# Kernel tuning notes

Measured on AMD Instinct MI355X. Metric: run time of the kernel, lower is better.

## Reference

```python
import jax, jax.numpy as jnp
from jax import lax
import numpy as np

# --- module constants (from init_kwargs) ---
MAXK = 512
BLOCK = 3            # Shi-Tomasi structure-tensor window
NUM_PAIRS = 256      # BAD descriptor dimensionality
ITERS = 20           # Sinkhorn iterations
EPS = 1.0            # entropy regularization
UNUSED = 1.0         # dustbin score
NMS_R = 3
THR = 0.0
PATCH_R = 8          # BAD pair-offset radius
BOX = 5              # BAD pre-smoothing box size

# fixed BAD comparison-pair offsets (dy1,dx1,dy2,dx2) -- constants, not learned
_OFFSETS = jnp.asarray(
    np.random.RandomState(42).randint(-PATCH_R, PATCH_R + 1, size=(NUM_PAIRS, 4)),
    dtype=jnp.int32)

_SOBEL_X = jnp.array([[-1., 0., 1.], [-2., 0., 2.], [-1., 0., 1.]], jnp.float32)[None, None]
_SOBEL_Y = jnp.transpose(_SOBEL_X, (0, 1, 3, 2))


def _conv(x, k):  # x: [B,1,H,W], k: [1,1,kh,kw]
    return lax.conv_general_dilated(x, k, (1, 1), 'SAME',
                                    dimension_numbers=('NCHW', 'OIHW', 'NCHW'))


def _detector(img):
    """Shi-Tomasi min-eigenvalue score map + dense BAD descriptor map."""
    Ix = _conv(img, _SOBEL_X)
    Iy = _conv(img, _SOBEL_Y)
    box = jnp.ones((1, 1, BLOCK, BLOCK), jnp.float32) / (BLOCK * BLOCK)
    Ixx = _conv(Ix * Ix, box)
    Iyy = _conv(Iy * Iy, box)
    Ixy = _conv(Ix * Iy, box)
    score = 0.5 * ((Ixx + Iyy) - jnp.sqrt((Ixx - Iyy) ** 2 + 4.0 * Ixy ** 2 + 1e-12))

    smooth = _conv(img, jnp.ones((1, 1, BOX, BOX), jnp.float32) / (BOX * BOX))[:, 0]  # [B,H,W]
    B, H, W = smooth.shape
    pad = jnp.pad(smooth, ((0, 0), (PATCH_R, PATCH_R), (PATCH_R, PATCH_R)), mode='edge')

    def one_pair(off):  # box-average difference at two shifted locations
        a = lax.dynamic_slice(pad, (0, PATCH_R + off[0], PATCH_R + off[1]), (B, H, W))
        b = lax.dynamic_slice(pad, (0, PATCH_R + off[2], PATCH_R + off[3]), (B, H, W))
        return a - b

    desc = jax.vmap(one_pair)(_OFFSETS)           # [D,B,H,W]
    return score[:, 0], jnp.transpose(desc, (1, 0, 2, 3))  # [B,H,W], [B,D,H,W]


def _nms_topk(score):
    """Max-pool NMS + top-k keypoint selection; invalid kpts = (-1,-1)."""
    win = 2 * NMS_R + 1
    mx = lax.reduce_window(score, -jnp.inf, lax.max, (1, win, win), (1, 1, 1), 'SAME')
    mask = (score >= mx) & (score > THR)
    B, H, W = score.shape
    masked = jnp.where(mask, score, -jnp.inf).reshape(B, H * W)
    vals, idx = lax.top_k(masked, MAXK)
    valid = jnp.isfinite(vals)
    y = (idx // W).astype(jnp.float32)
    x = (idx % W).astype(jnp.float32)
    kpts = jnp.where(valid[..., None], jnp.stack([y, x], -1), -1.0)  # [B,K,2] (y,x)
    return kpts


def _extract(desc_map, kpts):
    """Bilinear (subpixel) descriptor gather; zeros for invalid keypoints."""
    B, D, H, W = desc_map.shape
    valid = (kpts[:, :, 0] >= 0).astype(desc_map.dtype)
    y = jnp.clip(kpts[:, :, 0], 0.0, H - 1.0)
    x = jnp.clip(kpts[:, :, 1], 0.0, W - 1.0)
    y0 = jnp.floor(y); x0 = jnp.floor(x)
    y1 = jnp.minimum(y0 + 1.0, H - 1.0); x1 = jnp.minimum(x0 + 1.0, W - 1.0)
    wy = y - y0; wx = x - x0
    y0i, y1i = y0.astype(jnp.int32), y1.astype(jnp.int32)
    x0i, x1i = x0.astype(jnp.int32), x1.astype(jnp.int32)
    flat = desc_map.reshape(B, D, H * W)

    def g(yi, xi):  # [B,K] -> [B,D,K]
        return jnp.take_along_axis(flat, (yi * W + xi)[:, None, :], axis=2)

    d = (g(y0i, x0i) * ((1 - wy) * (1 - wx))[:, None, :]
         + g(y0i, x1i) * ((1 - wy) * wx)[:, None, :]
         + g(y1i, x0i) * (wy * (1 - wx))[:, None, :]
         + g(y1i, x1i) * (wy * wx)[:, None, :])
    return jnp.transpose(d, (0, 2, 1)) * valid[..., None]  # [B,K,D]


def _sinkhorn(d1, d2):
    """Log-domain Sinkhorn with dustbin row/col (SuperGlue-style OT)."""
    s1 = jnp.sum(d1 * d1, -1)
    s2 = jnp.sum(d2 * d2, -1)
    dist = jnp.sqrt(jnp.clip(
        s1[:, :, None] + s2[:, None, :] - 2.0 * jnp.einsum('bkd,bld->bkl', d1, d2),
        1e-12))
    B, K, _ = dist.shape
    Z = jnp.full((B, K + 1, K + 1), UNUSED / EPS, dtype=dist.dtype)
    Z = Z.at[:, :K, :K].set(-dist / EPS)
    norm = -jnp.log(2.0 * K)
    log_mu = jnp.concatenate([jnp.zeros((K,), Z.dtype),
                              jnp.log(jnp.full((1,), float(K), Z.dtype))]) + norm
    log_nu = log_mu

    def body(_, uv):
        u, v = uv
        u = log_mu - jax.scipy.special.logsumexp(Z + v[:, None, :], axis=2)
        v = log_nu - jax.scipy.special.logsumexp(Z + u[:, :, None], axis=1)
        return (u, v)

    u0 = jnp.zeros((B, K + 1), Z.dtype)
    u, v = lax.fori_loop(0, ITERS, body, (u0, u0))
    return jnp.exp(Z + u[:, :, None] + v[:, None, :] - norm)  # [B,K+1,K+1]


def _l2norm(d):
    return d / (jnp.linalg.norm(d, axis=-1, keepdims=True) + 1e-12)


def setup_inputs() -> dict:
    key = jax.random.key(0)
    k1, k2 = jax.random.split(key)
    image1 = jax.random.uniform(k1, (1, 1, 480, 640), jnp.float32)
    image2 = jax.random.uniform(k2, (1, 1, 480, 640), jnp.float32)
    return {"image1": image1, "image2": image2}


def reference(image1, image2):
    s1, m1 = _detector(image1)
    s2, m2 = _detector(image2)
    kpts1 = _nms_topk(s1)
    kpts2 = _nms_topk(s2)
    d1 = _l2norm(_extract(m1, kpts1))
    d2 = _l2norm(_extract(m2, kpts2))
    probs = _sinkhorn(d1, d2)
    return (kpts1, kpts2, probs)
```

## Files before the change

### kernel.cpp

```cpp
#include <hip/hip_runtime.h>
#include <math.h>
#include <stdint.h>

#define HH 480
#define WW 640
#define HW (HH*WW)
#define KK 512
#define DD 256
#define KP1 513
#define NSLOT 16
#define NBX 40
#define NBY 30
#define SLOTS_PER_IMG (NBX*NBY*NSLOT)
#define SVCAP 2048
#define SB 32
#define MU0 (1.0f/1024.0f)
#define MU1 (0.5f)
#define EDUST 2.71828182845904523536f

#define OFF_E      16384u
#define OFF_SMOOTH 2473984u
#define OFF_CAND   4931584u
#define OFF_KIDX   5238784u
#define OFF_DESC   5242880u
#define OFF_SBUF   6291456u
#define OFF_PC     6295552u
#define OFF_EU     6426880u

struct OffsTab { int v[1024]; };
static constexpr OffsTab make_offsets() {
  OffsTab o{};
  unsigned st[624] = {};
  st[0] = 42u;
  for (int i = 1; i < 624; ++i)
    st[i] = 1812433253u*(st[i-1] ^ (st[i-1] >> 30)) + (unsigned)i;
  int idx = 624, got = 0;
  while (got < 1024) {
    if (idx == 624) {
      for (int i = 0; i < 624; ++i) {
        unsigned y = (st[i] & 0x80000000u) | (st[(i+1)%624] & 0x7fffffffu);
        st[i] = st[(i+397)%624] ^ (y >> 1) ^ ((y & 1u) ? 2567483615u : 0u);
      }
      idx = 0;
    }
    unsigned y = st[idx++];
    y ^= y >> 11;
    y ^= (y << 7)  & 2636928640u;
    y ^= (y << 15) & 4022730752u;
    y ^= y >> 18;
    unsigned mv = y & 31u;
    if (mv <= 16u) { o.v[got] = (int)mv - 8; ++got; }
  }
  return o;
}
__device__ __constant__ OffsTab OFFS = make_offsets();

__global__ __launch_bounds__(256) void detnms_kernel(const float* __restrict__ img0,
    const float* __restrict__ img1, float* __restrict__ smooth,
    unsigned long long* __restrict__ cand) {
  __shared__ float tile[26][26];
  __shared__ float ixA[24][24], iyA[24][24];
  __shared__ float sc[22][22];
  __shared__ float vs[16][26];
  __shared__ float vm[16][22];
  __shared__ int wsum[4], wbase[4];
  const int imgI = blockIdx.z;
  const float* img = imgI ? img1 : img0;
  const int bx0 = blockIdx.x*16, by0 = blockIdx.y*16;
  const int tx = threadIdx.x, ty = threadIdx.y, lt = ty*16+tx;
  for (int p = lt; p < 676; p += 256) {
    int r = p/26, c = p%26;
    int gy = by0-5+r, gx = bx0-5+c;
    tile[r][c] = (gy >= 0 && gy < HH && gx >= 0 && gx < WW) ? img[gy*WW+gx] : 0.f;
  }
  __syncthreads();
  for (int p = lt; p < 576; p += 256) {
    int r = p/24, c = p%24;
    int gy = by0-4+r, gx = bx0-4+c;
    float ix = 0.f, iy = 0.f;
    if (gy >= 0 && gy < HH && gx >= 0 && gx < WW) {
      float t00 = tile[r][c],   t01 = tile[r][c+1],   t02 = tile[r][c+2];
      float t10 = tile[r+1][c],                        t12 = tile[r+1][c+2];
      float t20 = tile[r+2][c], t21 = tile[r+2][c+1], t22 = tile[r+2][c+2];
      ix = t00*(-1.f) + t02*1.f + t10*(-2.f) + t12*2.f + t20*(-1.f) + t22*1.f;
      iy = t00*(-1.f) + t01*(-2.f) + t02*(-1.f) + t20*1.f + t21*2.f + t22*1.f;
    }
    ixA[r][c] = ix; iyA[r][c] = iy;
  }
  __syncthreads();
  const float c9 = 1.f/9.f, c25 = 1.f/25.f;
  for (int p = lt; p < 484; p += 256) {
    int r = p/22, c = p%22;
    int gy = by0-3+r, gx = bx0-3+c;
    float v = -INFINITY;
    if (gy >= 0 && gy < HH && gx >= 0 && gx < WW) {
      float sxx = 0.f, syy = 0.f, sxy = 0.f;
      for (int dr = 0; dr < 3; ++dr)
        for (int dc = 0; dc < 3; ++dc) {
          float jx = ixA[r+dr][c+dc], jy = iyA[r+dr][c+dc];
          float pxxv = jx*jx, pyyv = jy*jy, pxyv = jx*jy;
          sxx += pxxv*c9; syy += pyyv*c9; sxy += pxyv*c9;
        }
      float tdif = sxx - syy;
      v = 0.5f * ((sxx + syy) - sqrtf(tdif*tdif + 4.f*(sxy*sxy) + 1e-12f));
    }
    sc[r][c] = v;
  }
  for (int p = lt; p < 416; p += 256) {
    int i = p/26, c = p%26;
    vs[i][c] = tile[i+3][c] + tile[i+4][c] + tile[i+5][c] + tile[i+6][c] + tile[i+7][c];
  }
  __syncthreads();
  for (int p = lt; p < 352; p += 256) {
    int i = p/22, c = p%22;
    float m = sc[i][c];
    m = fmaxf(m, sc[i+1][c]); m = fmaxf(m, sc[i+2][c]); m = fmaxf(m, sc[i+3][c]);
    m = fmaxf(m, sc[i+4][c]); m = fmaxf(m, sc[i+5][c]); m = fmaxf(m, sc[i+6][c]);
    vm[i][c] = m;
  }
  float sm = (vs[ty][tx+3] + vs[ty][tx+4] + vs[ty][tx+5] + vs[ty][tx+6] + vs[ty][tx+7]) * c25;
  smooth[imgI*HW + (by0+ty)*WW + (bx0+tx)] = sm;
  __syncthreads();
  float cv = sc[ty+3][tx+3];
  float m = vm[ty][tx];
  m = fmaxf(m, vm[ty][tx+1]); m = fmaxf(m, vm[ty][tx+2]); m = fmaxf(m, vm[ty][tx+3]);
  m = fmaxf(m, vm[ty][tx+4]); m = fmaxf(m, vm[ty][tx+5]); m = fmaxf(m, vm[ty][tx+6]);
  bool pred = (cv >= m && cv > 0.f);
  unsigned long long mask = __ballot(pred);
  int lane = lt & 63, wid = lt >> 6;
  if (lane == 0) wsum[wid] = __popcll(mask);
  __syncthreads();
  if (lt == 0) {
    int s0 = wsum[0], s1 = wsum[1], s2 = wsum[2], s3 = wsum[3];
    wbase[0] = 0; wbase[1] = s0; wbase[2] = s0+s1; wbase[3] = s0+s1+s2;
    wsum[0] = s0+s1+s2+s3;
  }
  __syncthreads();
  const int total = wsum[0];
  const size_t slotBase = (size_t)imgI*SLOTS_PER_IMG + (size_t)(blockIdx.y*NBX + blockIdx.x)*NSLOT;
  if (pred) {
    int pos = wbase[wid] + __popcll(mask & ((1ull << lane) - 1ull));
    if (pos < NSLOT) {
      int idx = (by0+ty)*WW + (bx0+tx);
      unsigned int ub = __float_as_uint(cv) | 0x80000000u;
      cand[slotBase + pos] = ((unsigned long long)ub << 32) | (unsigned int)(~idx);
    }
  }
  if (lt >= total && lt < NSLOT) cand[slotBase + lt] = 0ull;
}

__global__ __launch_bounds__(1024) void select2_kernel(const unsigned long long* __restrict__ cand,
    float* __restrict__ kptsOut, int* __restrict__ kidx) {
  __shared__ unsigned long long sk[SVCAP];
  __shared__ int hist[1024];
  __shared__ int sB1, sB2, sNeed, sCount;
  const int imgI = blockIdx.x, t = threadIdx.x;
  const unsigned long long* cd = cand + (size_t)imgI*SLOTS_PER_IMG;
  unsigned long long kreg[19];
  #pragma unroll
  for (int r = 0; r < 19; ++r) {
    int i = t + r*1024;
    kreg[r] = (i < SLOTS_PER_IMG) ? cd[i] : 0ull;
  }
  hist[t] = 0;
  if (t == 0) { sB1 = -1; sB2 = 0; sCount = 0; }
  __syncthreads();
  #pragma unroll
  for (int r = 0; r < 19; ++r)
    if (kreg[r]) atomicAdd(&hist[(int)(kreg[r] >> 54)], 1);
  __syncthreads();
  for (int d = 1; d < 1024; d <<= 1) {
    int vv = hist[t] + ((t + d < 1024) ? hist[t + d] : 0);
    __syncthreads();
    hist[t] = vv;
    __syncthreads();
  }
  if (hist[t] >= KK) atomicMax(&sB1, t);
  __syncthreads();
  const int b1 = sB1;
  if (t == 0 && b1 >= 0) sNeed = KK - ((b1 < 1023) ? hist[b1 + 1] : 0);
  __syncthreads();
  int b2 = 0;
  if (b1 >= 0) {
    hist[t] = 0;
    __syncthreads();
    #pragma unroll
    for (int r = 0; r < 19; ++r) {
      unsigned long long k = kreg[r];
      if (k && (int)(k >> 54) == b1) atomicAdd(&hist[(int)(k >> 44) & 1023], 1);
    }
    __syncthreads();
    for (int d = 1; d < 1024; d <<= 1) {
      int vv = hist[t] + ((t + d < 1024) ? hist[t + d] : 0);
      __syncthreads();
      hist[t] = vv;
      __syncthreads();
    }
    if (hist[t] >= sNeed) atomicMax(&sB2, t);
    __syncthreads();
    b2 = sB2;
  }
  #pragma unroll
  for (int r = 0; r < 19; ++r) {
    unsigned long long k = kreg[r];
    if (k) {
      int bin1 = (int)(k >> 54);
      if (bin1 > b1 || (bin1 == b1 && ((int)(k >> 44) & 1023) >= b2)) {
        int pos = atomicAdd(&sCount, 1);
        if (pos < SVCAP) sk[pos] = k;
      }
    }
  }
  __syncthreads();
  const int n = (sCount < SVCAP) ? sCount : SVCAP;
  for (int k = n + t; k < KK; k += 1024) {
    kptsOut[imgI*2*KK + 2*k]     = -1.f;
    kptsOut[imgI*2*KK + 2*k + 1] = -1.f;
    kidx[imgI*KK + k] = -1;
  }
  for (int i = t; i < n; i += 1024) {
    unsigned long long key = sk[i];
    int r = 0;
    for (int m = 0; m < n; ++m) r += (sk[m] > key) ? 1 : 0;
    if (r < KK) {
      int id = (int)(~(unsigned int)(key & 0xFFFFFFFFull));
      kptsOut[imgI*2*KK + 2*r]     = (float)(id / WW);
      kptsOut[imgI*2*KK + 2*r + 1] = (float)(id % WW);
      kidx[imgI*KK + r] = id;
    }
  }
}

__global__ __launch_bounds__(256) void desc_kernel(const float* __restrict__ smooth,
    const int* __restrict__ kidx, float* __restrict__ desc, float* __restrict__ sbuf) {
  __shared__ float wsum[4];
  const int k = blockIdx.x, imgI = blockIdx.y;
  const int j = threadIdx.x;
  const int id = kidx[imgI*KK + k];
  float val = 0.f;
  if (id >= 0) {
    int y = id / WW, x = id % WW;
    int o0 = OFFS.v[4*j], o1 = OFFS.v[4*j+1], o2 = OFFS.v[4*j+2], o3 = OFFS.v[4*j+3];
    const float* sm = smooth + imgI*HW;
    int ya = min(max(y+o0, 0), HH-1), xa = min(max(x+o1, 0), WW-1);
    int yb = min(max(y+o2, 0), HH-1), xb = min(max(x+o3, 0), WW-1);
    val = sm[ya*WW + xa] - sm[yb*WW + xb];
  }
  float ss = val*val;
  for (int off = 32; off; off >>= 1) ss += __shfl_down(ss, off);
  if ((j & 63) == 0) wsum[j >> 6] = ss;
  __syncthreads();
  if (j == 0) wsum[0] = wsum[0] + wsum[1] + wsum[2] + wsum[3];
  __syncthreads();
  float tot = wsum[0];
  float inv = 1.f / (sqrtf(tot) + 1e-12f);
  desc[((size_t)imgI*KK + k)*DD + j] = val * inv;
  if (j == 0) sbuf[imgI*KK + k] = tot * inv * inv;
}

__global__ __launch_bounds__(256) void zbuild_kernel(const float* __restrict__ desc,
    const float* __restrict__ sbuf, float* __restrict__ E) {
  __shared__ float sA[32][260], sB[32][260];
  const int ty = threadIdx.y, tx = threadIdx.x;
  const int i0 = blockIdx.y*32, j0 = blockIdx.x*32;
  const int lt = ty*16 + tx;
  for (int p = lt; p < 32*DD; p += 256) {
    int r = p >> 8, c = p & 255;
    sA[r][c] = desc[((size_t)(i0 + r))*DD + c];
    sB[r][c] = desc[((size_t)(KK + j0 + r))*DD + c];
  }
  __syncthreads();
  const float4* pa0 = (const float4*)&sA[ty][0];
  const float4* pa1 = (const float4*)&sA[ty+16][0];
  const float4* pb0 = (const float4*)&sB[tx][0];
  const float4* pb1 = (const float4*)&sB[tx+16][0];
  float a00 = 0.f, a01 = 0.f, a10 = 0.f, a11 = 0.f;
  for (int c4 = 0; c4 < DD/4; ++c4) {
    float4 a0 = pa0[c4], a1 = pa1[c4], b0 = pb0[c4], b1 = pb1[c4];
    a00 += a0.x*b0.x; a00 += a0.y*b0.y; a00 += a0.z*b0.z; a00 += a0.w*b0.w;
    a01 += a0.x*b1.x; a01 += a0.y*b1.y; a01 += a0.z*b1.z; a01 += a0.w*b1.w;
    a10 += a1.x*b0.x; a10 += a1.y*b0.y; a10 += a1.z*b0.z; a10 += a1.w*b0.w;
    a11 += a1.x*b1.x; a11 += a1.y*b1.y; a11 += a1.z*b1.z; a11 += a1.w*b1.w;
  }
  const float s0 = sbuf[i0 + ty], s0b = sbuf[i0 + ty + 16];
  const float s1 = sbuf[KK + j0 + tx], s1b = sbuf[KK + j0 + tx + 16];
  E[(size_t)(i0+ty)   *KK + j0+tx]    = expf(-sqrtf(fmaxf(s0  + s1  - 2.f*a00, 1e-12f)));
  E[(size_t)(i0+ty)   *KK + j0+tx+16] = expf(-sqrtf(fmaxf(s0  + s1b - 2.f*a01, 1e-12f)));
  E[(size_t)(i0+ty+16)*KK + j0+tx]    = expf(-sqrtf(fmaxf(s0b + s1  - 2.f*a10, 1e-12f)));
  E[(size_t)(i0+ty+16)*KK + j0+tx+16] = expf(-sqrtf(fmaxf(s0b + s1b - 2.f*a11, 1e-12f)));
}

__global__ __launch_bounds__(1024) void sink_step_kernel(const float* __restrict__ E,
    const float* __restrict__ PcolIn, float* __restrict__ PcolOut,
    float* __restrict__ euBuf, float* __restrict__ probs, int mode) {
  __shared__ float ev[KP1];
  __shared__ float pcolw[16][520];
  const int t = threadIdx.x, b = blockIdx.x;
  const int widx = t >> 6, lane = t & 63;
  const int r = b*16 + widx;
  const int j0 = lane*8;
  if (mode == 0) {
    for (int j = t; j < KP1; j += 1024) ev[j] = 1.f;
  } else {
    for (int j = t; j < KP1; j += 1024) {
      float s = 0.f;
      #pragma unroll
      for (int w = 0; w < SB; ++w) s += PcolIn[w*KP1 + j];
      float nu = (j < KK) ? MU0 : MU1;
      ev[j] = nu / s;
    }
  }
  __syncthreads();
  float4 va = *(const float4*)&ev[j0];
  float4 vb = *(const float4*)&ev[j0+4];
  float evv[8] = {va.x,va.y,va.z,va.w,vb.x,vb.y,vb.z,vb.w};
  const float ev512 = ev[512];
  const float* er = E + (size_t)r*KK;
  float4 e0 = *(const float4*)&er[j0];
  float4 e1 = *(const float4*)&er[j0+4];
  float ee[8] = {e0.x,e0.y,e0.z,e0.w,e1.x,e1.y,e1.z,e1.w};
  if (mode == 2) {
    const float euR = euBuf[r];
    float* pr = probs + (size_t)r*KP1;
    #pragma unroll
    for (int q = 0; q < 8; ++q) pr[j0+q] = ee[q] * euR * evv[q] * 1024.f;
    if (lane == 0) pr[512] = EDUST * euR * ev512 * 1024.f;
    if (r == 511) {
      const float euD = euBuf[512];
      float* pd = probs + (size_t)512*KP1;
      #pragma unroll
      for (int q = 0; q < 8; ++q) pd[j0+q] = EDUST * euD * evv[q] * 1024.f;
      if (lane == 0) pd[512] = EDUST * euD * ev512 * 1024.f;
    }
    return;
  }
  float S = 0.f;
  #pragma unroll
  for (int q = 0; q < 8; ++q) S += ee[q] * evv[q];
  if (lane == 0) S += EDUST * ev512;
  #pragma unroll
  for (int off = 32; off; off >>= 1) S += __shfl_xor(S, off);
  const float euR = MU0 / S;
  if (lane == 0) euBuf[r] = euR;
  float pacc[8];
  #pragma unroll
  for (int q = 0; q < 8; ++q) pacc[q] = ee[q] * euR;
  float pacc8 = EDUST * euR;
  if (r == 511) {
    float Sd = 0.f;
    #pragma unroll
    for (int q = 0; q < 8; ++q) Sd += evv[q];
    if (lane == 0) Sd += ev512;
    #pragma unroll
    for (int off = 32; off; off >>= 1) Sd += __shfl_xor(Sd, off);
    Sd *= EDUST;
    const float euD = MU1 / Sd;
    if (lane == 0) euBuf[512] = euD;
    #pragma unroll
    for (int q = 0; q < 8; ++q) pacc[q] += EDUST * euD;
    pacc8 += EDUST * euD;
  }
  *(float4*)&pcolw[widx][j0]   = make_float4(pacc[0], pacc[1], pacc[2], pacc[3]);
  *(float4*)&pcolw[widx][j0+4] = make_float4(pacc[4], pacc[5], pacc[6], pacc[7]);
  if (lane == 0) pcolw[widx][512] = pacc8;
  __syncthreads();
  float* pc = PcolOut + b*KP1;
  for (int j = t; j < KP1; j += 1024) {
    float s = 0.f;
    #pragma unroll
    for (int w = 0; w < 16; ++w) s += pcolw[w][j];
    pc[j] = s;
  }
}

extern "C" void kernel_launch(void* const* d_in, const int* in_sizes, int n_in,
                              void* d_out, int out_size, void* d_ws, size_t ws_size,
                              hipStream_t stream) {
  const float* img1 = (const float*)d_in[0];
  const float* img2 = (const float*)d_in[1];
  float* out = (float*)d_out;
  char* ws = (char*)d_ws;

  float* smooth = (float*)(ws + OFF_SMOOTH);
  unsigned long long* cand = (unsigned long long*)(ws + OFF_CAND);
  int*   kidx   = (int*)  (ws + OFF_KIDX);
  float* desc   = (float*)(ws + OFF_DESC);
  float* sbuf   = (float*)(ws + OFF_SBUF);
  float* E      = (float*)(ws + OFF_E);
  float* pcA    = (float*)(ws + OFF_PC);
  float* pcB    = (float*)(ws + OFF_PC) + SB*KP1;
  float* euBuf  = (float*)(ws + OFF_EU);
  float* probsOut = out + 2*KK*2;

  detnms_kernel<<<dim3(NBX, NBY, 2), dim3(16, 16), 0, stream>>>(img1, img2, smooth, cand);
  select2_kernel<<<2, 1024, 0, stream>>>(cand, out, kidx);
  desc_kernel<<<dim3(KK, 2), 256, 0, stream>>>(smooth, kidx, desc, sbuf);
  zbuild_kernel<<<dim3(16, 16), dim3(16, 16), 0, stream>>>(desc, sbuf, E);

  sink_step_kernel<<<SB, 1024, 0, stream>>>(E, pcB, pcA, euBuf, probsOut, 0);
  int ping = 0;
  for (int it = 1; it < 20; ++it) {
    float* pin  = ping ? pcB : pcA;
    float* pout = ping ? pcA : pcB;
    sink_step_kernel<<<SB, 1024, 0, stream>>>(E, pin, pout, euBuf, probsOut, 1);
    ping ^= 1;
  }
  {
    float* pin = ping ? pcB : pcA;
    sink_step_kernel<<<SB, 1024, 0, stream>>>(E, pin, pcA, euBuf, probsOut, 2);
  }
}
```

Measured before the change: 138.5 us.

## Enlarge detector tiles to 32x32 and process two rows per Sinkhorn wave

The detector/NMS kernel now covers a 32x32 output tile per 256-thread block, with each thread handling four pixels. This cuts halo overhead and the block count, while keeping the 16x16 candidate sub-tile slot layout through four sequential ballot/compaction rounds. The Sinkhorn step kernel now has each wavefront handle two rows of E, so it launches 16 blocks instead of 32 and each column-sum step reads half as many partial-sum rows. The trade-off is more extra syncs in the detector and fewer active CUs in the Sinkhorn steps.

```diff
diff --git a/kernel.cpp b/kernel.cpp
--- a/kernel.cpp
+++ b/kernel.cpp
@@ -13,7 +13,7 @@
 #define NBY 30
 #define SLOTS_PER_IMG (NBX*NBY*NSLOT)
 #define SVCAP 2048
-#define SB 32
+#define SBK 16
 #define MU0 (1.0f/1024.0f)
 #define MU1 (0.5f)
 #define EDUST 2.71828182845904523536f
@@ -58,24 +58,24 @@
 __global__ __launch_bounds__(256) void detnms_kernel(const float* __restrict__ img0,
     const float* __restrict__ img1, float* __restrict__ smooth,
     unsigned long long* __restrict__ cand) {
-  __shared__ float tile[26][26];
-  __shared__ float ixA[24][24], iyA[24][24];
-  __shared__ float sc[22][22];
-  __shared__ float vs[16][26];
-  __shared__ float vm[16][22];
+  __shared__ float tile[42][42];
+  __shared__ float ixA[40][40], iyA[40][40];
+  __shared__ float sc[38][38];
+  __shared__ float vs[32][42];
+  __shared__ float vm[32][38];
   __shared__ int wsum[4], wbase[4];
   const int imgI = blockIdx.z;
   const float* img = imgI ? img1 : img0;
-  const int bx0 = blockIdx.x*16, by0 = blockIdx.y*16;
+  const int bx0 = blockIdx.x*32, by0 = blockIdx.y*32;
   const int tx = threadIdx.x, ty = threadIdx.y, lt = ty*16+tx;
-  for (int p = lt; p < 676; p += 256) {
-    int r = p/26, c = p%26;
+  for (int p = lt; p < 1764; p += 256) {
+    int r = p/42, c = p%42;
     int gy = by0-5+r, gx = bx0-5+c;
     tile[r][c] = (gy >= 0 && gy < HH && gx >= 0 && gx < WW) ? img[gy*WW+gx] : 0.f;
   }
   __syncthreads();
-  for (int p = lt; p < 576; p += 256) {
-    int r = p/24, c = p%24;
+  for (int p = lt; p < 1600; p += 256) {
+    int r = p/40, c = p%40;
     int gy = by0-4+r, gx = bx0-4+c;
     float ix = 0.f, iy = 0.f;
     if (gy >= 0 && gy < HH && gx >= 0 && gx < WW) {
@@ -89,8 +89,8 @@
   }
   __syncthreads();
   const float c9 = 1.f/9.f, c25 = 1.f/25.f;
-  for (int p = lt; p < 484; p += 256) {
-    int r = p/22, c = p%22;
+  for (int p = lt; p < 1444; p += 256) {
+    int r = p/38, c = p%38;
     int gy = by0-3+r, gx = bx0-3+c;
     float v = -INFINITY;
     if (gy >= 0 && gy < HH && gx >= 0 && gx < WW) {
@@ -106,47 +106,64 @@
     }
     sc[r][c] = v;
   }
-  for (int p = lt; p < 416; p += 256) {
-    int i = p/26, c = p%26;
+  for (int p = lt; p < 1344; p += 256) {
+    int i = p/42, c = p%42;
     vs[i][c] = tile[i+3][c] + tile[i+4][c] + tile[i+5][c] + tile[i+6][c] + tile[i+7][c];
   }
   __syncthreads();
-  for (int p = lt; p < 352; p += 256) {
-    int i = p/22, c = p%22;
+  for (int p = lt; p < 1216; p += 256) {
+    int i = p/38, c = p%38;
     float m = sc[i][c];
     m = fmaxf(m, sc[i+1][c]); m = fmaxf(m, sc[i+2][c]); m = fmaxf(m, sc[i+3][c]);
     m = fmaxf(m, sc[i+4][c]); m = fmaxf(m, sc[i+5][c]); m = fmaxf(m, sc[i+6][c]);
     vm[i][c] = m;
   }
-  float sm = (vs[ty][tx+3] + vs[ty][tx+4] + vs[ty][tx+5] + vs[ty][tx+6] + vs[ty][tx+7]) * c25;
-  smooth[imgI*HW + (by0+ty)*WW + (bx0+tx)] = sm;
-  __syncthreads();
-  float cv = sc[ty+3][tx+3];
-  float m = vm[ty][tx];
-  m = fmaxf(m, vm[ty][tx+1]); m = fmaxf(m, vm[ty][tx+2]); m = fmaxf(m, vm[ty][tx+3]);
-  m = fmaxf(m, vm[ty][tx+4]); m = fmaxf(m, vm[ty][tx+5]); m = fmaxf(m, vm[ty][tx+6]);
-  bool pred = (cv >= m && cv > 0.f);
-  unsigned long long mask = __ballot(pred);
-  int lane = lt & 63, wid = lt >> 6;
-  if (lane == 0) wsum[wid] = __popcll(mask);
-  __syncthreads();
-  if (lt == 0) {
-    int s0 = wsum[0], s1 = wsum[1], s2 = wsum[2], s3 = wsum[3];
-    wbase[0] = 0; wbase[1] = s0; wbase[2] = s0+s1; wbase[3] = s0+s1+s2;
-    wsum[0] = s0+s1+s2+s3;
-  }
-  __syncthreads();
-  const int total = wsum[0];
-  const size_t slotBase = (size_t)imgI*SLOTS_PER_IMG + (size_t)(blockIdx.y*NBX + blockIdx.x)*NSLOT;
-  if (pred) {
-    int pos = wbase[wid] + __popcll(mask & ((1ull << lane) - 1ull));
-    if (pos < NSLOT) {
-      int idx = (by0+ty)*WW + (bx0+tx);
-      unsigned int ub = __float_as_uint(cv) | 0x80000000u;
-      cand[slotBase + pos] = ((unsigned long long)ub << 32) | (unsigned int)(~idx);
-    }
-  }
-  if (lt >= total && lt < NSLOT) cand[slotBase + lt] = 0ull;
+  #pragma unroll
+  for (int q = 0; q < 4; ++q) {
+    int py = ty + 16*(q >> 1), px = tx + 16*(q & 1);
+    float sm = (vs[py][px+3] + vs[py][px+4] + vs[py][px+5] + vs[py][px+6] + vs[py][px+7]) * c25;
+    smooth[imgI*HW + (by0+py)*WW + (bx0+px)] = sm;
+  }
+  __syncthreads();
+  bool pred[4]; float cvv[4];
+  #pragma unroll
+  for (int q = 0; q < 4; ++q) {
+    int py = ty + 16*(q >> 1), px = tx + 16*(q & 1);
+    float cv = sc[py+3][px+3];
+    float m = vm[py][px];
+    m = fmaxf(m, vm[py][px+1]); m = fmaxf(m, vm[py][px+2]); m = fmaxf(m, vm[py][px+3]);
+    m = fmaxf(m, vm[py][px+4]); m = fmaxf(m, vm[py][px+5]); m = fmaxf(m, vm[py][px+6]);
+    pred[q] = (cv >= m && cv > 0.f);
+    cvv[q] = cv;
+  }
+  const int lane = lt & 63, wid = lt >> 6;
+  #pragma unroll
+  for (int q = 0; q < 4; ++q) {
+    unsigned long long mask = __ballot(pred[q]);
+    if (lane == 0) wsum[wid] = __popcll(mask);
+    __syncthreads();
+    if (lt == 0) {
+      int s0 = wsum[0], s1 = wsum[1], s2 = wsum[2], s3 = wsum[3];
+      wbase[0] = 0; wbase[1] = s0; wbase[2] = s0+s1; wbase[3] = s0+s1+s2;
+      wsum[0] = s0+s1+s2+s3;
+    }
+    __syncthreads();
+    const int total = wsum[0];
+    const int a = q >> 1, b = q & 1;
+    const int subTile = (blockIdx.y*2 + a)*NBX + (blockIdx.x*2 + b);
+    const size_t slotBase = (size_t)imgI*SLOTS_PER_IMG + (size_t)subTile*NSLOT;
+    if (pred[q]) {
+      int pos = wbase[wid] + __popcll(mask & ((1ull << lane) - 1ull));
+      if (pos < NSLOT) {
+        int py = ty + 16*a, px = tx + 16*b;
+        int idx = (by0+py)*WW + (bx0+px);
+        unsigned int ub = __float_as_uint(cvv[q]) | 0x80000000u;
+        cand[slotBase + pos] = ((unsigned long long)ub << 32) | (unsigned int)(~idx);
+      }
+    }
+    if (lt >= total && lt < NSLOT) cand[slotBase + lt] = 0ull;
+    __syncthreads();
+  }
 }
 
 __global__ __launch_bounds__(1024) void select2_kernel(const unsigned long long* __restrict__ cand,
@@ -297,15 +314,17 @@
   __shared__ float pcolw[16][520];
   const int t = threadIdx.x, b = blockIdx.x;
   const int widx = t >> 6, lane = t & 63;
-  const int r = b*16 + widx;
+  const int gw = b*16 + widx;
   const int j0 = lane*8;
+  const int r0 = 2*gw, r1 = 2*gw + 1;
+  const bool hasDust = (gw == 255);
   if (mode == 0) {
     for (int j = t; j < KP1; j += 1024) ev[j] = 1.f;
   } else {
     for (int j = t; j < KP1; j += 1024) {
       float s = 0.f;
       #pragma unroll
-      for (int w = 0; w < SB; ++w) s += PcolIn[w*KP1 + j];
+      for (int w = 0; w < SBK; ++w) s += PcolIn[w*KP1 + j];
       float nu = (j < KK) ? MU0 : MU1;
       ev[j] = nu / s;
     }
@@ -315,17 +334,28 @@
   float4 vb = *(const float4*)&ev[j0+4];
   float evv[8] = {va.x,va.y,va.z,va.w,vb.x,vb.y,vb.z,vb.w};
   const float ev512 = ev[512];
-  const float* er = E + (size_t)r*KK;
-  float4 e0 = *(const float4*)&er[j0];
-  float4 e1 = *(const float4*)&er[j0+4];
-  float ee[8] = {e0.x,e0.y,e0.z,e0.w,e1.x,e1.y,e1.z,e1.w};
+  const float* er0 = E + (size_t)r0*KK;
+  const float* er1 = E + (size_t)r1*KK;
+  float4 e00 = *(const float4*)&er0[j0];
+  float4 e01 = *(const float4*)&er0[j0+4];
+  float4 e10 = *(const float4*)&er1[j0];
+  float4 e11 = *(const float4*)&er1[j0+4];
+  float ee0[8] = {e00.x,e00.y,e00.z,e00.w,e01.x,e01.y,e01.z,e01.w};
+  float ee1[8] = {e10.x,e10.y,e10.z,e10.w,e11.x,e11.y,e11.z,e11.w};
   if (mode == 2) {
-    const float euR = euBuf[r];
-    float* pr = probs + (size_t)r*KP1;
-    #pragma unroll
-    for (int q = 0; q < 8; ++q) pr[j0+q] = ee[q] * euR * evv[q] * 1024.f;
-    if (lane == 0) pr[512] = EDUST * euR * ev512 * 1024.f;
-    if (r == 511) {
+    const float eu0 = euBuf[r0], eu1 = euBuf[r1];
+    float* pr0 = probs + (size_t)r0*KP1;
+    float* pr1 = probs + (size_t)r1*KP1;
+    #pragma unroll
+    for (int q = 0; q < 8; ++q) {
+      pr0[j0+q] = ee0[q] * eu0 * evv[q] * 1024.f;
+      pr1[j0+q] = ee1[q] * eu1 * evv[q] * 1024.f;
+    }
+    if (lane == 0) {
+      pr0[512] = EDUST * eu0 * ev512 * 1024.f;
+      pr1[512] = EDUST * eu1 * ev512 * 1024.f;
+    }
+    if (hasDust) {
       const float euD = euBuf[512];
       float* pd = probs + (size_t)512*KP1;
       #pragma unroll
@@ -334,19 +364,22 @@
     }
     return;
   }
-  float S = 0.f;
-  #pragma unroll
-  for (int q = 0; q < 8; ++q) S += ee[q] * evv[q];
-  if (lane == 0) S += EDUST * ev512;
-  #pragma unroll
-  for (int off = 32; off; off >>= 1) S += __shfl_xor(S, off);
-  const float euR = MU0 / S;
-  if (lane == 0) euBuf[r] = euR;
+  float S0 = 0.f, S1 = 0.f;
+  #pragma unroll
+  for (int q = 0; q < 8; ++q) { S0 += ee0[q] * evv[q]; S1 += ee1[q] * evv[q]; }
+  if (lane == 0) { S0 += EDUST * ev512; S1 += EDUST * ev512; }
+  #pragma unroll
+  for (int off = 32; off; off >>= 1) {
+    S0 += __shfl_xor(S0, off);
+    S1 += __shfl_xor(S1, off);
+  }
+  const float eu0 = MU0 / S0, eu1 = MU0 / S1;
+  if (lane == 0) { euBuf[r0] = eu0; euBuf[r1] = eu1; }
   float pacc[8];
   #pragma unroll
-  for (int q = 0; q < 8; ++q) pacc[q] = ee[q] * euR;
-  float pacc8 = EDUST * euR;
-  if (r == 511) {
+  for (int q = 0; q < 8; ++q) pacc[q] = ee0[q] * eu0 + ee1[q] * eu1;
+  float pacc8 = EDUST * eu0 + EDUST * eu1;
+  if (hasDust) {
     float Sd = 0.f;
     #pragma unroll
     for (int q = 0; q < 8; ++q) Sd += evv[q];
@@ -388,25 +421,25 @@
   float* sbuf   = (float*)(ws + OFF_SBUF);
   float* E      = (float*)(ws + OFF_E);
   float* pcA    = (float*)(ws + OFF_PC);
-  float* pcB    = (float*)(ws + OFF_PC) + SB*KP1;
+  float* pcB    = (float*)(ws + OFF_PC) + SBK*KP1;
   float* euBuf  = (float*)(ws + OFF_EU);
   float* probsOut = out + 2*KK*2;
 
-  detnms_kernel<<<dim3(NBX, NBY, 2), dim3(16, 16), 0, stream>>>(img1, img2, smooth, cand);
+  detnms_kernel<<<dim3(20, 15, 2), dim3(16, 16), 0, stream>>>(img1, img2, smooth, cand);
   select2_kernel<<<2, 1024, 0, stream>>>(cand, out, kidx);
   desc_kernel<<<dim3(KK, 2), 256, 0, stream>>>(smooth, kidx, desc, sbuf);
   zbuild_kernel<<<dim3(16, 16), dim3(16, 16), 0, stream>>>(desc, sbuf, E);
 
-  sink_step_kernel<<<SB, 1024, 0, stream>>>(E, pcB, pcA, euBuf, probsOut, 0);
+  sink_step_kernel<<<SBK, 1024, 0, stream>>>(E, pcB, pcA, euBuf, probsOut, 0);
   int ping = 0;
   for (int it = 1; it < 20; ++it) {
     float* pin  = ping ? pcB : pcA;
     float* pout = ping ? pcA : pcB;
-    sink_step_kernel<<<SB, 1024, 0, stream>>>(E, pin, pout, euBuf, probsOut, 1);
+    sink_step_kernel<<<SBK, 1024, 0, stream>>>(E, pin, pout, euBuf, probsOut, 1);
     ping ^= 1;
   }
   {
     float* pin = ping ? pcB : pcA;
-    sink_step_kernel<<<SB, 1024, 0, stream>>>(E, pin, pcA, euBuf, probsOut, 2);
-  }
-}
+    sink_step_kernel<<<SBK, 1024, 0, stream>>>(E, pin, pcA, euBuf, probsOut, 2);
+  }
+}
```

Result: no change. 140.1 us (median of 2 runs) (+1.1%).
